# Performance work log

Hardware: AMD Instinct MI355X
Metric: run time of the kernel (lower is better)

The kernel has to match this reference:

```python
import jax, jax.numpy as jnp
import numpy as np

B, S, E = 2, 2048, 1024
H = 16
DK = E // H          # 64
ROT_DIM = 32         # min(32, embed_dim)
THETA = 10000.0


def _rope_tables(seq_len, dtype):
    # lucidrains RotaryEmbedding: inv_freq over even indices, repeated pairwise
    inv_freq = 1.0 / (THETA ** (jnp.arange(0, ROT_DIM, 2, dtype=jnp.float32) / ROT_DIM))
    t = jnp.arange(seq_len, dtype=jnp.float32)
    freqs = t[:, None] * inv_freq[None, :]            # [S, ROT_DIM/2]
    freqs = jnp.repeat(freqs, 2, axis=-1)             # [S, ROT_DIM] (interleaved repeat)
    return jnp.cos(freqs).astype(dtype), jnp.sin(freqs).astype(dtype)


def _rotate_half(x):
    # interleaved pairs: (x1, x2) -> (-x2, x1)
    x1 = x[..., 0::2]
    x2 = x[..., 1::2]
    return jnp.stack([-x2, x1], axis=-1).reshape(x.shape)


def _apply_rope(x, cos, sin):
    # x: [B, H, S, DK]; rotate first ROT_DIM dims, pass through the rest
    xr, xp = x[..., :ROT_DIM], x[..., ROT_DIM:]
    xr = xr * cos + _rotate_half(xr) * sin
    return jnp.concatenate([xr, xp], axis=-1)


def setup_inputs() -> dict:
    rng = jax.random.key(0)
    ks = jax.random.split(rng, 9)
    bound = 1.0 / np.sqrt(E)
    inp = {
        "query": jax.random.normal(ks[0], (B, S, E), dtype=jnp.float32),
        "key": jax.random.normal(ks[1], (B, S, E), dtype=jnp.float32),
        "value": jax.random.normal(ks[2], (B, S, E), dtype=jnp.float32),
        "Wq": jax.random.uniform(ks[3], (E, E), jnp.float32, -bound, bound),
        "bq": jax.random.uniform(ks[4], (E,), jnp.float32, -bound, bound),
        "Wk": jax.random.uniform(ks[5], (E, E), jnp.float32, -bound, bound),
        "bk": jax.random.uniform(ks[6], (E,), jnp.float32, -bound, bound),
        "Wv": jax.random.uniform(ks[7], (E, E), jnp.float32, -bound, bound),
        "bv": jax.random.uniform(ks[8], (E,), jnp.float32, -bound, bound),
    }
    return inp


def reference(query, key, value, Wq, bq, Wk, bk, Wv, bv):
    b, s, _ = query.shape
    # separate QKV linears (torch Linear: x @ W.T + b)
    q = query @ Wq.T + bq
    k = key @ Wk.T + bk
    v = value @ Wv.T + bv
    # [B, S, E] -> [B, H, S, DK]
    q = q.reshape(b, s, H, DK).transpose(0, 2, 1, 3)
    k = k.reshape(b, s, H, DK).transpose(0, 2, 1, 3)
    v = v.reshape(b, s, H, DK).transpose(0, 2, 1, 3)
    # rotary embedding on query and key
    cos, sin = _rope_tables(s, q.dtype)
    q = _apply_rope(q, cos, sin)
    k = _apply_rope(k, cos, sin)
    # scaled dot-product attention (no mask)
    scores = jnp.einsum('bhqd,bhkd->bhqk', q, k) / jnp.sqrt(jnp.asarray(DK, q.dtype))
    attn = jax.nn.softmax(scores, axis=-1)
    x = jnp.einsum('bhqk,bhkd->bhqd', attn, v)
    x = x.transpose(0, 2, 1, 3).reshape(b, s, H * DK)
    return (x, attn)
```

## Files before the change

### kernel.cpp

```cpp
#include <hip/hip_runtime.h>
#include <hip/hip_bf16.h>

#define B_  2
#define S_  2048
#define E_  1024
#define H_  16
#define DK_ 64
#define BH_ (B_*H_)
#define M_  (B_*S_)

typedef __attribute__((ext_vector_type(8))) short bf16x8;
typedef __attribute__((ext_vector_type(4))) float f32x4;
typedef unsigned short u16;
typedef unsigned int   u32;

__device__ __forceinline__ float bf2f(u16 u) {
    u32 x = ((u32)u) << 16;
    float f;
    __builtin_memcpy(&f, &x, 4);
    return f;
}
__device__ __forceinline__ u16 f2bf(float f) {
    u32 x;
    __builtin_memcpy(&x, &f, 4);
    u32 r = (x + 0x7fffu + ((x >> 16) & 1u)) >> 16;
    return (u16)r;
}

__device__ __forceinline__ void stage8f(u16* dst, const float* src) {
    float4 f0 = *(const float4*)src;
    float4 f1 = *(const float4*)(src + 4);
    u16 tmp[8] = {f2bf(f0.x), f2bf(f0.y), f2bf(f0.z), f2bf(f0.w),
                  f2bf(f1.x), f2bf(f1.y), f2bf(f1.z), f2bf(f1.w)};
    *(uint4*)dst = *(uint4*)tmp;
}
__device__ __forceinline__ void store8f(float* dst, const u16* src) {
    bf16x8 v = *(const bf16x8*)src;
    float4 lo = {bf2f((u16)v[0]), bf2f((u16)v[1]), bf2f((u16)v[2]), bf2f((u16)v[3])};
    float4 hi = {bf2f((u16)v[4]), bf2f((u16)v[5]), bf2f((u16)v[6]), bf2f((u16)v[7])};
    *(float4*)dst       = lo;
    *(float4*)(dst + 4) = hi;
}

__global__ void probe_kernel(const u16* __restrict__ w, int* __restrict__ flag)
{
    if (threadIdx.x == 0 && blockIdx.x == 0) {
        int big = 0;
        for (int i = 0; i < 128; i++) {
            float v = bf2f(w[i]);
            if (fabsf(v) > 0.25f) big++;
        }
        *flag = (big >= 4) ? 1 : 0;
    }
}

__global__ __launch_bounds__(256) void proj_kernel(
    const void* __restrict__ Xv, const void* __restrict__ Wv,
    const void* __restrict__ biasv, u16* __restrict__ out, int vmode,
    const int* __restrict__ flag)
{
    __shared__ __align__(16) u16 als[64*72];
    __shared__ __align__(16) u16 bls[64*72];
    const int isf32 = *flag;
    const int t    = threadIdx.x;
    const int m0   = blockIdx.x * 64;
    const int n0   = blockIdx.y * 64;
    const int w    = t >> 6;
    const int ln   = t & 15;
    const int quad = (t >> 4) & 3;
    const int lr   = t >> 3;
    const int c8   = (t & 7) * 8;

    f32x4 acc[4];
    #pragma unroll
    for (int i = 0; i < 4; i++) acc[i] = (f32x4){0.f, 0.f, 0.f, 0.f};

    for (int kt = 0; kt < E_; kt += 64) {
        __syncthreads();
        if (isf32) {
            const float* Xf = (const float*)Xv;
            const float* Wf = (const float*)Wv;
            stage8f(&als[lr*72 + c8],      &Xf[(size_t)(m0+lr)*E_    + kt + c8]);
            stage8f(&als[(lr+32)*72 + c8], &Xf[(size_t)(m0+lr+32)*E_ + kt + c8]);
            stage8f(&bls[lr*72 + c8],      &Wf[(size_t)(n0+lr)*E_    + kt + c8]);
            stage8f(&bls[(lr+32)*72 + c8], &Wf[(size_t)(n0+lr+32)*E_ + kt + c8]);
        } else {
            const u16* X = (const u16*)Xv;
            const u16* W = (const u16*)Wv;
            *(uint4*)&als[lr*72 + c8]      = *(const uint4*)&X[(size_t)(m0+lr)*E_    + kt + c8];
            *(uint4*)&als[(lr+32)*72 + c8] = *(const uint4*)&X[(size_t)(m0+lr+32)*E_ + kt + c8];
            *(uint4*)&bls[lr*72 + c8]      = *(const uint4*)&W[(size_t)(n0+lr)*E_    + kt + c8];
            *(uint4*)&bls[(lr+32)*72 + c8] = *(const uint4*)&W[(size_t)(n0+lr+32)*E_ + kt + c8];
        }
        __syncthreads();
        #pragma unroll
        for (int c = 0; c < 2; c++) {
            bf16x8 a = *(const bf16x8*)&als[(w*16+ln)*72 + c*32 + quad*8];
            #pragma unroll
            for (int cb = 0; cb < 4; cb++) {
                bf16x8 b = *(const bf16x8*)&bls[(cb*16+ln)*72 + c*32 + quad*8];
                acc[cb] = __builtin_amdgcn_mfma_f32_16x16x32_bf16(a, b, acc[cb], 0, 0, 0);
            }
        }
    }

    #pragma unroll
    for (int cb = 0; cb < 4; cb++) {
        const int n  = n0 + cb*16 + ln;
        const float bv = isf32 ? ((const float*)biasv)[n] : bf2f(((const u16*)biasv)[n]);
        const int h = n >> 6;
        const int d = n & 63;
        #pragma unroll
        for (int r = 0; r < 4; r++) {
            const int m  = m0 + w*16 + quad*4 + r;
            const int bb = m >> 11;
            const int s  = m & (S_ - 1);
            const float v = acc[cb][r] + bv;
            size_t addr;
            if (vmode == 0) addr = (((size_t)(bb*H_ + h))*S_  + s)*DK_ + d;
            else            addr = (((size_t)(bb*H_ + h))*DK_ + d)*S_  + s;
            out[addr] = f2bf(v);
        }
    }
}

__global__ __launch_bounds__(256) void rope_kernel(u16* __restrict__ qw, u16* __restrict__ kw)
{
    const int t   = threadIdx.x;
    const int pos = blockIdx.x * 8 + (t >> 5);
    const int j   = t & 31;
    const int isq = (blockIdx.y == 0);
    u16* base = (isq ? qw : kw) + (size_t)pos * DK_;
    const int s = pos & (S_ - 1);
    const float scale = isq ? 0.125f : 1.0f;
    if (j < 16) {
        const float invf = powf(10000.0f, -(float)(2*j) / 32.0f);
        const float ang  = (float)s * invf;
        float sn, cs;
        sincosf(ang, &sn, &cs);
        const float x0 = bf2f(base[2*j]);
        const float x1 = bf2f(base[2*j+1]);
        base[2*j]   = f2bf((x0*cs - x1*sn) * scale);
        base[2*j+1] = f2bf((x1*cs + x0*sn) * scale);
    } else if (isq) {
        const int d = j + 16;
        base[d]      = f2bf(bf2f(base[d])      * 0.125f);
        base[d+16]   = f2bf(bf2f(base[d+16])   * 0.125f);
    }
}

__global__ __launch_bounds__(256) void attn_kernel(
    const u16* __restrict__ qw, const u16* __restrict__ kw, const u16* __restrict__ vw,
    void* __restrict__ outbase, const int* __restrict__ flag)
{
    __shared__ __align__(16) u16 qls[64*72];
    __shared__ __align__(16) u16 kls[64*72];
    __shared__ __align__(16) u16 vls[64*72];
    __shared__ __align__(16) u16 pls[64*72];

    const int isf32 = *flag;
    const int t    = threadIdx.x;
    const int q0   = blockIdx.x * 64;
    const int bh   = blockIdx.y;
    const int w    = t >> 6;
    const int ln   = t & 15;
    const int quad = (t >> 4) & 3;
    const int lr   = t >> 3;
    const int c8   = (t & 7) * 8;

    const u16* qb = qw + (size_t)bh * S_ * DK_;
    const u16* kb = kw + (size_t)bh * S_ * DK_;
    const u16* vb = vw + (size_t)bh * DK_ * S_;

    *(uint4*)&qls[lr*72 + c8]      = *(const uint4*)&qb[(size_t)(q0+lr)*DK_    + c8];
    *(uint4*)&qls[(lr+32)*72 + c8] = *(const uint4*)&qb[(size_t)(q0+lr+32)*DK_ + c8];

    float rs[4] = {0.f, 0.f, 0.f, 0.f};
    for (int kt = 0; kt < S_; kt += 64) {
        __syncthreads();
        *(uint4*)&kls[lr*72 + c8]      = *(const uint4*)&kb[(size_t)(kt+lr)*DK_    + c8];
        *(uint4*)&kls[(lr+32)*72 + c8] = *(const uint4*)&kb[(size_t)(kt+lr+32)*DK_ + c8];
        __syncthreads();
        f32x4 sc[4];
        #pragma unroll
        for (int i = 0; i < 4; i++) sc[i] = (f32x4){0.f, 0.f, 0.f, 0.f};
        #pragma unroll
        for (int c = 0; c < 2; c++) {
            bf16x8 a = *(const bf16x8*)&qls[(w*16+ln)*72 + c*32 + quad*8];
            #pragma unroll
            for (int cb = 0; cb < 4; cb++) {
                bf16x8 b = *(const bf16x8*)&kls[(cb*16+ln)*72 + c*32 + quad*8];
                sc[cb] = __builtin_amdgcn_mfma_f32_16x16x32_bf16(a, b, sc[cb], 0, 0, 0);
            }
        }
        #pragma unroll
        for (int cb = 0; cb < 4; cb++)
            #pragma unroll
            for (int r = 0; r < 4; r++)
                rs[r] += expf(fminf(sc[cb][r], 60.0f));
    }
    #pragma unroll
    for (int r = 0; r < 4; r++) {
        rs[r] += __shfl_xor(rs[r], 1, 64);
        rs[r] += __shfl_xor(rs[r], 2, 64);
        rs[r] += __shfl_xor(rs[r], 4, 64);
        rs[r] += __shfl_xor(rs[r], 8, 64);
    }
    float inv[4];
    #pragma unroll
    for (int r = 0; r < 4; r++) inv[r] = 1.0f / rs[r];

    f32x4 xacc[4];
    #pragma unroll
    for (int i = 0; i < 4; i++) xacc[i] = (f32x4){0.f, 0.f, 0.f, 0.f};

    for (int kt = 0; kt < S_; kt += 64) {
        __syncthreads();
        *(uint4*)&kls[lr*72 + c8]      = *(const uint4*)&kb[(size_t)(kt+lr)*DK_    + c8];
        *(uint4*)&kls[(lr+32)*72 + c8] = *(const uint4*)&kb[(size_t)(kt+lr+32)*DK_ + c8];
        *(uint4*)&vls[lr*72 + c8]      = *(const uint4*)&vb[(size_t)lr*S_      + kt + c8];
        *(uint4*)&vls[(lr+32)*72 + c8] = *(const uint4*)&vb[(size_t)(lr+32)*S_ + kt + c8];
        __syncthreads();
        f32x4 sc[4];
        #pragma unroll
        for (int i = 0; i < 4; i++) sc[i] = (f32x4){0.f, 0.f, 0.f, 0.f};
        #pragma unroll
        for (int c = 0; c < 2; c++) {
            bf16x8 a = *(const bf16x8*)&qls[(w*16+ln)*72 + c*32 + quad*8];
            #pragma unroll
            for (int cb = 0; cb < 4; cb++) {
                bf16x8 b = *(const bf16x8*)&kls[(cb*16+ln)*72 + c*32 + quad*8];
                sc[cb] = __builtin_amdgcn_mfma_f32_16x16x32_bf16(a, b, sc[cb], 0, 0, 0);
            }
        }
        #pragma unroll
        for (int cb = 0; cb < 4; cb++)
            #pragma unroll
            for (int r = 0; r < 4; r++) {
                const float p = expf(fminf(sc[cb][r], 60.0f)) * inv[r];
                pls[(w*16 + quad*4 + r)*72 + cb*16 + ln] = f2bf(p);
            }
        __syncthreads();
        {
            const size_t a0 = ((size_t)bh*S_ + (q0+lr))*S_ + kt + c8;
            const size_t a1 = ((size_t)bh*S_ + (q0+lr+32))*S_ + kt + c8;
            if (isf32) {
                float* af = (float*)outbase + (size_t)M_*E_;
                store8f(&af[a0], &pls[lr*72 + c8]);
                store8f(&af[a1], &pls[(lr+32)*72 + c8]);
            } else {
                u16* au = (u16*)outbase + (size_t)M_*E_;
                *(uint4*)&au[a0] = *(const uint4*)&pls[lr*72 + c8];
                *(uint4*)&au[a1] = *(const uint4*)&pls[(lr+32)*72 + c8];
            }
        }
        #pragma unroll
        for (int c = 0; c < 2; c++) {
            bf16x8 a = *(const bf16x8*)&pls[(w*16+ln)*72 + c*32 + quad*8];
            #pragma unroll
            for (int cb = 0; cb < 4; cb++) {
                bf16x8 b = *(const bf16x8*)&vls[(cb*16+ln)*72 + c*32 + quad*8];
                xacc[cb] = __builtin_amdgcn_mfma_f32_16x16x32_bf16(a, b, xacc[cb], 0, 0, 0);
            }
        }
    }

    const int bb = bh >> 4;
    const int h  = bh & 15;
    #pragma unroll
    for (int cb = 0; cb < 4; cb++) {
        const int d = cb*16 + ln;
        #pragma unroll
        for (int r = 0; r < 4; r++) {
            const int s = q0 + w*16 + quad*4 + r;
            const size_t idx = (((size_t)bb*S_ + s)*H_ + h)*DK_ + d;
            if (isf32) ((float*)outbase)[idx] = xacc[cb][r];
            else       ((u16*)outbase)[idx]   = f2bf(xacc[cb][r]);
        }
    }
}

extern "C" void kernel_launch(void* const* d_in, const int* in_sizes, int n_in,
                              void* d_out, int out_size, void* d_ws, size_t ws_size,
                              hipStream_t stream)
{
    const void* query = d_in[0];
    const void* key   = d_in[1];
    const void* value = d_in[2];
    const void* Wq    = d_in[3];
    const void* bq    = d_in[4];
    const void* Wk    = d_in[5];
    const void* bk    = d_in[6];
    const void* Wv    = d_in[7];
    const void* bv    = d_in[8];

    int* flag = (int*)d_ws;
    u16* qws  = (u16*)((char*)d_ws + 64);
    u16* kws  = qws + (size_t)M_ * E_;
    u16* vws  = kws + (size_t)M_ * E_;

    probe_kernel<<<1, 64, 0, stream>>>((const u16*)Wq, flag);

    dim3 gp(M_/64, E_/64);
    proj_kernel<<<gp, 256, 0, stream>>>(query, Wq, bq, qws, 0, flag);
    proj_kernel<<<gp, 256, 0, stream>>>(key,   Wk, bk, kws, 0, flag);
    proj_kernel<<<gp, 256, 0, stream>>>(value, Wv, bv, vws, 1, flag);
    rope_kernel<<<dim3(BH_*S_/8, 2), 256, 0, stream>>>(qws, kws);
    attn_kernel<<<dim3(S_/64, BH_), 256, 0, stream>>>(qws, kws, vws, d_out, flag);
}
```

Measured before the change: 865.3 us.

## Pre-convert inputs to bf16, enlarge projection tiles, use async LDS loads with swizzle

Adds a conversion kernel that turns the fp32 activations and weights into bf16 workspace copies before the projections. The projection GEMM now uses 128x128 tiles with 4x4 MFMA fragments per wave, loaded through global_load_lds direct-to-LDS copies into an XOR-swizzled layout. The attention kernel also uses async swizzled K/V loads, keeps Q fragments in registers, and remaps block IDs to group work across XCDs. The aim is to cut redundant fp32 conversion, raise data reuse in the GEMMs and reduce LDS bank conflicts. The cost is an extra pass over the inputs, more workspace and higher register pressure.

New measurement: 868.2 us. Within noise of the previous version (+0.3%).

```diff
diff --git a/kernel.cpp b/kernel.cpp
--- a/kernel.cpp
+++ b/kernel.cpp
@@ -27,13 +27,15 @@
     return (u16)r;
 }
 
-__device__ __forceinline__ void stage8f(u16* dst, const float* src) {
-    float4 f0 = *(const float4*)src;
-    float4 f1 = *(const float4*)(src + 4);
-    u16 tmp[8] = {f2bf(f0.x), f2bf(f0.y), f2bf(f0.z), f2bf(f0.w),
-                  f2bf(f1.x), f2bf(f1.y), f2bf(f1.z), f2bf(f1.w)};
-    *(uint4*)dst = *(uint4*)tmp;
-}
+__device__ __forceinline__ void async16(const void* g, void* l) {
+    __builtin_amdgcn_global_load_lds(
+        (__attribute__((address_space(1))) void*)(g),
+        (__attribute__((address_space(3))) void*)(l), 16, 0, 0);
+}
+__device__ __forceinline__ bf16x8 frag_at(const u16* base, int byteoff) {
+    return *(const bf16x8*)((const char*)base + byteoff);
+}
+
 __device__ __forceinline__ void store8f(float* dst, const u16* src) {
     bf16x8 v = *(const bf16x8*)src;
     float4 lo = {bf2f((u16)v[0]), bf2f((u16)v[1]), bf2f((u16)v[2]), bf2f((u16)v[3])};
@@ -54,72 +56,109 @@
     }
 }
 
+__global__ __launch_bounds__(256) void convert_kernel(
+    const void* __restrict__ q, const void* __restrict__ k, const void* __restrict__ v,
+    const void* __restrict__ wq, const void* __restrict__ wk, const void* __restrict__ wv,
+    u16* __restrict__ dq, u16* __restrict__ dk, u16* __restrict__ dv,
+    u16* __restrict__ ewq, u16* __restrict__ ewk, u16* __restrict__ ewv,
+    const int* __restrict__ flag)
+{
+    const int y = blockIdx.y;
+    const void* src; u16* dst; size_t n;
+    switch (y) {
+        case 0: src = q;  dst = dq;  n = (size_t)M_*E_; break;
+        case 1: src = k;  dst = dk;  n = (size_t)M_*E_; break;
+        case 2: src = v;  dst = dv;  n = (size_t)M_*E_; break;
+        case 3: src = wq; dst = ewq; n = (size_t)E_*E_; break;
+        case 4: src = wk; dst = ewk; n = (size_t)E_*E_; break;
+        default:src = wv; dst = ewv; n = (size_t)E_*E_; break;
+    }
+    const size_t i = ((size_t)blockIdx.x * 256 + threadIdx.x) * 8;
+    if (i >= n) return;
+    if (*flag) {
+        const float* s = (const float*)src + i;
+        float4 f0 = *(const float4*)s;
+        float4 f1 = *(const float4*)(s + 4);
+        u16 tmp[8] = {f2bf(f0.x), f2bf(f0.y), f2bf(f0.z), f2bf(f0.w),
+                      f2bf(f1.x), f2bf(f1.y), f2bf(f1.z), f2bf(f1.w)};
+        *(uint4*)(dst + i) = *(uint4*)tmp;
+    } else {
+        *(uint4*)(dst + i) = *(const uint4*)((const u16*)src + i);
+    }
+}
+
 __global__ __launch_bounds__(256) void proj_kernel(
-    const void* __restrict__ Xv, const void* __restrict__ Wv,
+    const u16* __restrict__ X, const u16* __restrict__ W,
     const void* __restrict__ biasv, u16* __restrict__ out, int vmode,
     const int* __restrict__ flag)
 {
-    __shared__ __align__(16) u16 als[64*72];
-    __shared__ __align__(16) u16 bls[64*72];
+    __shared__ __align__(16) u16 als[128*64];
+    __shared__ __align__(16) u16 bls[128*64];
     const int isf32 = *flag;
     const int t    = threadIdx.x;
-    const int m0   = blockIdx.x * 64;
-    const int n0   = blockIdx.y * 64;
     const int w    = t >> 6;
     const int ln   = t & 15;
     const int quad = (t >> 4) & 3;
-    const int lr   = t >> 3;
-    const int c8   = (t & 7) * 8;
-
-    f32x4 acc[4];
-    #pragma unroll
-    for (int i = 0; i < 4; i++) acc[i] = (f32x4){0.f, 0.f, 0.f, 0.f};
+    const int wr   = w >> 1;
+    const int wc   = w & 1;
+    const int m0   = blockIdx.x * 128;
+    const int n0   = blockIdx.y * 128;
+    const int l    = t & 63;
+    const int srow = l >> 3;
+    const int scsw = ((l & 7) * 16) ^ (srow << 4);
+    const int rxor = (ln & 7) << 4;
+
+    f32x4 acc[4][4];
+    #pragma unroll
+    for (int i = 0; i < 4; i++)
+        #pragma unroll
+        for (int j = 0; j < 4; j++) acc[i][j] = (f32x4){0.f, 0.f, 0.f, 0.f};
 
     for (int kt = 0; kt < E_; kt += 64) {
         __syncthreads();
-        if (isf32) {
-            const float* Xf = (const float*)Xv;
-            const float* Wf = (const float*)Wv;
-            stage8f(&als[lr*72 + c8],      &Xf[(size_t)(m0+lr)*E_    + kt + c8]);
-            stage8f(&als[(lr+32)*72 + c8], &Xf[(size_t)(m0+lr+32)*E_ + kt + c8]);
-            stage8f(&bls[lr*72 + c8],      &Wf[(size_t)(n0+lr)*E_    + kt + c8]);
-            stage8f(&bls[(lr+32)*72 + c8], &Wf[(size_t)(n0+lr+32)*E_ + kt + c8]);
-        } else {
-            const u16* X = (const u16*)Xv;
-            const u16* W = (const u16*)Wv;
-            *(uint4*)&als[lr*72 + c8]      = *(const uint4*)&X[(size_t)(m0+lr)*E_    + kt + c8];
-            *(uint4*)&als[(lr+32)*72 + c8] = *(const uint4*)&X[(size_t)(m0+lr+32)*E_ + kt + c8];
-            *(uint4*)&bls[lr*72 + c8]      = *(const uint4*)&W[(size_t)(n0+lr)*E_    + kt + c8];
-            *(uint4*)&bls[(lr+32)*72 + c8] = *(const uint4*)&W[(size_t)(n0+lr+32)*E_ + kt + c8];
+        #pragma unroll
+        for (int j = 0; j < 4; j++) {
+            const int rowa = w*32 + j*8;
+            async16(&X[(size_t)(m0 + rowa + srow)*E_ + kt + (scsw >> 1)], &als[rowa*64]);
+            async16(&W[(size_t)(n0 + rowa + srow)*E_ + kt + (scsw >> 1)], &bls[rowa*64]);
         }
         __syncthreads();
         #pragma unroll
         for (int c = 0; c < 2; c++) {
-            bf16x8 a = *(const bf16x8*)&als[(w*16+ln)*72 + c*32 + quad*8];
-            #pragma unroll
-            for (int cb = 0; cb < 4; cb++) {
-                bf16x8 b = *(const bf16x8*)&bls[(cb*16+ln)*72 + c*32 + quad*8];
-                acc[cb] = __builtin_amdgcn_mfma_f32_16x16x32_bf16(a, b, acc[cb], 0, 0, 0);
-            }
-        }
-    }
-
-    #pragma unroll
-    for (int cb = 0; cb < 4; cb++) {
-        const int n  = n0 + cb*16 + ln;
+            const int koff = c*64 + quad*16;
+            bf16x8 a[4];
+            #pragma unroll
+            for (int mf = 0; mf < 4; mf++)
+                a[mf] = frag_at(als, (wr*64 + mf*16 + ln)*128 + (koff ^ rxor));
+            #pragma unroll
+            for (int nf = 0; nf < 4; nf++) {
+                bf16x8 b = frag_at(bls, (wc*64 + nf*16 + ln)*128 + (koff ^ rxor));
+                #pragma unroll
+                for (int mf = 0; mf < 4; mf++)
+                    acc[mf][nf] = __builtin_amdgcn_mfma_f32_16x16x32_bf16(a[mf], b, acc[mf][nf], 0, 0, 0);
+            }
+        }
+    }
+
+    #pragma unroll
+    for (int nf = 0; nf < 4; nf++) {
+        const int n  = n0 + wc*64 + nf*16 + ln;
         const float bv = isf32 ? ((const float*)biasv)[n] : bf2f(((const u16*)biasv)[n]);
         const int h = n >> 6;
         const int d = n & 63;
         #pragma unroll
-        for (int r = 0; r < 4; r++) {
-            const int m  = m0 + w*16 + quad*4 + r;
-            const int bb = m >> 11;
-            const int s  = m & (S_ - 1);
-            const float v = acc[cb][r] + bv;
-            size_t addr;
-            if (vmode == 0) addr = (((size_t)(bb*H_ + h))*S_  + s)*DK_ + d;
-            else            addr = (((size_t)(bb*H_ + h))*DK_ + d)*S_  + s;
-            out[addr] = f2bf(v);
+        for (int mf = 0; mf < 4; mf++) {
+            #pragma unroll
+            for (int r = 0; r < 4; r++) {
+                const int m  = m0 + wr*64 + mf*16 + quad*4 + r;
+                const int bb = m >> 11;
+                const int s  = m & (S_ - 1);
+                const float v = acc[mf][nf][r] + bv;
+                size_t addr;
+                if (vmode == 0) addr = (((size_t)(bb*H_ + h))*S_  + s)*DK_ + d;
+                else            addr = (((size_t)(bb*H_ + h))*DK_ + d)*S_  + s;
+                out[addr] = f2bf(v);
+            }
         }
     }
 }
@@ -154,19 +193,25 @@
     void* __restrict__ outbase, const int* __restrict__ flag)
 {
     __shared__ __align__(16) u16 qls[64*72];
-    __shared__ __align__(16) u16 kls[64*72];
-    __shared__ __align__(16) u16 vls[64*72];
     __shared__ __align__(16) u16 pls[64*72];
+    __shared__ __align__(16) u16 kls[64*64];
+    __shared__ __align__(16) u16 vls[64*64];
 
     const int isf32 = *flag;
     const int t    = threadIdx.x;
-    const int q0   = blockIdx.x * 64;
-    const int bh   = blockIdx.y;
+    const int id   = blockIdx.y * gridDim.x + blockIdx.x;
+    const int nid  = (id & 7) * 128 + (id >> 3);
+    const int bh   = nid >> 5;
+    const int q0   = (nid & 31) * 64;
     const int w    = t >> 6;
     const int ln   = t & 15;
     const int quad = (t >> 4) & 3;
     const int lr   = t >> 3;
     const int c8   = (t & 7) * 8;
+    const int l    = t & 63;
+    const int srow = l >> 3;
+    const int scsw = ((l & 7) * 16) ^ (srow << 4);
+    const int rxor = (ln & 7) << 4;
 
     const u16* qb = qw + (size_t)bh * S_ * DK_;
     const u16* kb = kw + (size_t)bh * S_ * DK_;
@@ -174,23 +219,31 @@
 
     *(uint4*)&qls[lr*72 + c8]      = *(const uint4*)&qb[(size_t)(q0+lr)*DK_    + c8];
     *(uint4*)&qls[(lr+32)*72 + c8] = *(const uint4*)&qb[(size_t)(q0+lr+32)*DK_ + c8];
+    __syncthreads();
+    bf16x8 qa[2];
+    #pragma unroll
+    for (int c = 0; c < 2; c++)
+        qa[c] = *(const bf16x8*)&qls[(w*16+ln)*72 + c*32 + quad*8];
 
     float rs[4] = {0.f, 0.f, 0.f, 0.f};
     for (int kt = 0; kt < S_; kt += 64) {
         __syncthreads();
-        *(uint4*)&kls[lr*72 + c8]      = *(const uint4*)&kb[(size_t)(kt+lr)*DK_    + c8];
-        *(uint4*)&kls[(lr+32)*72 + c8] = *(const uint4*)&kb[(size_t)(kt+lr+32)*DK_ + c8];
+        #pragma unroll
+        for (int j = 0; j < 2; j++) {
+            const int rowa = w*16 + j*8;
+            async16(&kb[(size_t)(kt + rowa + srow)*DK_ + (scsw >> 1)], &kls[rowa*64]);
+        }
         __syncthreads();
         f32x4 sc[4];
         #pragma unroll
         for (int i = 0; i < 4; i++) sc[i] = (f32x4){0.f, 0.f, 0.f, 0.f};
         #pragma unroll
         for (int c = 0; c < 2; c++) {
-            bf16x8 a = *(const bf16x8*)&qls[(w*16+ln)*72 + c*32 + quad*8];
+            const int koff = c*64 + quad*16;
             #pragma unroll
             for (int cb = 0; cb < 4; cb++) {
-                bf16x8 b = *(const bf16x8*)&kls[(cb*16+ln)*72 + c*32 + quad*8];
-                sc[cb] = __builtin_amdgcn_mfma_f32_16x16x32_bf16(a, b, sc[cb], 0, 0, 0);
+                bf16x8 b = frag_at(kls, (cb*16+ln)*128 + (koff ^ rxor));
+                sc[cb] = __builtin_amdgcn_mfma_f32_16x16x32_bf16(qa[c], b, sc[cb], 0, 0, 0);
             }
         }
         #pragma unroll
@@ -216,21 +269,23 @@
 
     for (int kt = 0; kt < S_; kt += 64) {
         __syncthreads();
-        *(uint4*)&kls[lr*72 + c8]      = *(const uint4*)&kb[(size_t)(kt+lr)*DK_    + c8];
-        *(uint4*)&kls[(lr+32)*72 + c8] = *(const uint4*)&kb[(size_t)(kt+lr+32)*DK_ + c8];
-        *(uint4*)&vls[lr*72 + c8]      = *(const uint4*)&vb[(size_t)lr*S_      + kt + c8];
-        *(uint4*)&vls[(lr+32)*72 + c8] = *(const uint4*)&vb[(size_t)(lr+32)*S_ + kt + c8];
+        #pragma unroll
+        for (int j = 0; j < 2; j++) {
+            const int rowa = w*16 + j*8;
+            async16(&kb[(size_t)(kt + rowa + srow)*DK_ + (scsw >> 1)], &kls[rowa*64]);
+            async16(&vb[(size_t)(rowa + srow)*S_ + kt + (scsw >> 1)],  &vls[rowa*64]);
+        }
         __syncthreads();
         f32x4 sc[4];
         #pragma unroll
         for (int i = 0; i < 4; i++) sc[i] = (f32x4){0.f, 0.f, 0.f, 0.f};
         #pragma unroll
         for (int c = 0; c < 2; c++) {
-            bf16x8 a = *(const bf16x8*)&qls[(w*16+ln)*72 + c*32 + quad*8];
+            const int koff = c*64 + quad*16;
             #pragma unroll
             for (int cb = 0; cb < 4; cb++) {
-                bf16x8 b = *(const bf16x8*)&kls[(cb*16+ln)*72 + c*32 + quad*8];
-                sc[cb] = __builtin_amdgcn_mfma_f32_16x16x32_bf16(a, b, sc[cb], 0, 0, 0);
+                bf16x8 b = frag_at(kls, (cb*16+ln)*128 + (koff ^ rxor));
+                sc[cb] = __builtin_amdgcn_mfma_f32_16x16x32_bf16(qa[c], b, sc[cb], 0, 0, 0);
             }
         }
         #pragma unroll
@@ -256,11 +311,12 @@
         }
         #pragma unroll
         for (int c = 0; c < 2; c++) {
-            bf16x8 a = *(const bf16x8*)&pls[(w*16+ln)*72 + c*32 + quad*8];
+            const int koff = c*64 + quad*16;
+            bf16x8 pa = *(const bf16x8*)&pls[(w*16+ln)*72 + c*32 + quad*8];
             #pragma unroll
             for (int cb = 0; cb < 4; cb++) {
-                bf16x8 b = *(const bf16x8*)&vls[(cb*16+ln)*72 + c*32 + quad*8];
-                xacc[cb] = __builtin_amdgcn_mfma_f32_16x16x32_bf16(a, b, xacc[cb], 0, 0, 0);
+                bf16x8 b = frag_at(vls, (cb*16+ln)*128 + (koff ^ rxor));
+                xacc[cb] = __builtin_amdgcn_mfma_f32_16x16x32_bf16(pa, b, xacc[cb], 0, 0, 0);
             }
         }
     }
@@ -298,13 +354,21 @@
     u16* qws  = (u16*)((char*)d_ws + 64);
     u16* kws  = qws + (size_t)M_ * E_;
     u16* vws  = kws + (size_t)M_ * E_;
+    u16* xq   = vws + (size_t)M_ * E_;
+    u16* xk   = xq  + (size_t)M_ * E_;
+    u16* xv   = xk  + (size_t)M_ * E_;
+    u16* wqc  = xv  + (size_t)M_ * E_;
+    u16* wkc  = wqc + (size_t)E_ * E_;
+    u16* wvc  = wkc + (size_t)E_ * E_;
 
     probe_kernel<<<1, 64, 0, stream>>>((const u16*)Wq, flag);
-
-    dim3 gp(M_/64, E_/64);
-    proj_kernel<<<gp, 256, 0, stream>>>(query, Wq, bq, qws, 0, flag);
-    proj_kernel<<<gp, 256, 0, stream>>>(key,   Wk, bk, kws, 0, flag);
-    proj_kernel<<<gp, 256, 0, stream>>>(value, Wv, bv, vws, 1, flag);
+    convert_kernel<<<dim3(2048, 6), 256, 0, stream>>>(
+        query, key, value, Wq, Wk, Wv, xq, xk, xv, wqc, wkc, wvc, flag);
+
+    dim3 gp(M_/128, E_/128);
+    proj_kernel<<<gp, 256, 0, stream>>>(xq, wqc, bq, qws, 0, flag);
+    proj_kernel<<<gp, 256, 0, stream>>>(xk, wkc, bk, kws, 0, flag);
+    proj_kernel<<<gp, 256, 0, stream>>>(xv, wvc, bv, vws, 1, flag);
     rope_kernel<<<dim3(BH_*S_/8, 2), 256, 0, stream>>>(qws, kws);
     attn_kernel<<<dim3(S_/64, BH_), 256, 0, stream>>>(qws, kws, vws, d_out, flag);
 }
```
